# Kernel optimization log

Measured on AMD Instinct MI355X. Metric: run time of the kernel, lower is better.

Reference implementation:

```python
import jax, jax.numpy as jnp
import numpy as np

N_KERNELS = 11
B, Q, D, E, C = 128, 32, 512, 300, 128

def _kernel_mus(n):
    mus = [1.0]
    bs = 2.0 / (n - 1)
    mus.append(1 - bs / 2)
    for i in range(1, n - 1):
        mus.append(mus[i] - bs)
    return np.array(mus, dtype=np.float32)

def _kernel_sigmas(n):
    bs = 2.0 / (n - 1)
    return np.array([0.001] + [0.5 * bs] * (n - 1), dtype=np.float32)

def setup_inputs():
    key = jax.random.key(0)
    ks = jax.random.split(key, 10)
    return {
        "query_embeddings": jax.random.normal(ks[0], (B, Q, E), jnp.float32),
        "document_embeddings": jax.random.normal(ks[1], (B, D, E), jnp.float32),
        "query_pad_oov_mask": jnp.ones((B, Q), jnp.float32),
        "document_pad_oov_mask": jnp.ones((B, D), jnp.float32),
        "conv1_w": jax.random.normal(ks[2], (C, E, 1), jnp.float32) * 0.05,
        "conv1_b": jnp.zeros((C,), jnp.float32),
        "conv2_w": jax.random.normal(ks[3], (C, E, 2), jnp.float32) * 0.05,
        "conv2_b": jnp.zeros((C,), jnp.float32),
        "conv3_w": jax.random.normal(ks[4], (C, E, 3), jnp.float32) * 0.05,
        "conv3_b": jnp.zeros((C,), jnp.float32),
        "nn_scaler": jnp.full((1,), 0.01, jnp.float32),
        "dense_w": jax.random.uniform(ks[5], (1, N_KERNELS * 9), jnp.float32, -0.014, 0.014),
        "dense_b": jnp.zeros((1,), jnp.float32),
        "dense_mean_w": jax.random.normal(ks[6], (1, N_KERNELS * 9), jnp.float32) * 0.05,
        "dense_mean_b": jnp.zeros((1,), jnp.float32),
        "dense_comb_w": jax.random.normal(ks[7], (1, 2), jnp.float32) * 0.5,
    }

def _conv_relu(x, w, b):
    # x: [B, L, E] -> [B, L, C]; right-pad by k-1 (ConstantPad1d((0, k-1))) so out len == L
    k = w.shape[-1]
    y = jax.lax.conv_general_dilated(x.transpose(0, 2, 1), w, (1,), [(0, k - 1)],
                                     dimension_numbers=("NCH", "OIH", "NCH"))
    return jax.nn.relu(y + b[None, :, None]).transpose(0, 2, 1)

def _kernel_pool(q, d, qd_mask, q_mask, doc_len, mu, sigma, scaler):
    # cosine matrix (AllenNLP CosineMatrixAttention: L2-normalize with 1e-13 tie-break)
    qn = q / (jnp.linalg.norm(q, axis=-1, keepdims=True) + 1e-13)
    dn = d / (jnp.linalg.norm(d, axis=-1, keepdims=True) + 1e-13)
    cos = jnp.einsum("bqc,bdc->bqd", qn, dn) * qd_mask
    # RBF soft-histogram kernels over the similarity matrix: [B,q,d,K]
    kr = jnp.exp(-(cos[..., None] - mu) ** 2 / (2.0 * sigma ** 2)) * qd_mask[..., None]
    pkq = kr.sum(axis=2)  # [B, Q, K]
    std = (jnp.log(jnp.clip(pkq, 1e-10)) * scaler * q_mask[..., None]).sum(axis=1)
    pkq_mean = pkq / doc_len[:, None, None]
    mean = (jnp.log(jnp.clip(pkq_mean, 1e-10)) * scaler * q_mask[..., None]).sum(axis=1)
    return std, mean

def _forward(qe, de, qm, dm, c1w, c1b, c2w, c2b, c3w, c3b, ns, dw, db, dmw, dmb, dcw):
    mu = jnp.asarray(_kernel_mus(N_KERNELS))
    sigma = jnp.asarray(_kernel_sigmas(N_KERNELS))
    qd_mask = qm[:, :, None] * dm[:, None, :]
    doc_len = dm.sum(axis=1)
    convs = [(c1w, c1b), (c2w, c2b), (c3w, c3b)]
    q_res = [_conv_relu(qe, w, b) for w, b in convs]
    d_res = [_conv_relu(de, w, b) for w, b in convs]
    std_list, mean_list = [], []
    for qr in q_res:
        for dr in d_res:
            s, m = _kernel_pool(qr, dr, qd_mask, qm, doc_len, mu, sigma, ns)
            std_list.append(s)
            mean_list.append(m)
    all_grams = jnp.concatenate(std_list, axis=1)       # [B, 9*K]
    all_grams_mean = jnp.concatenate(mean_list, axis=1)
    dense_out = all_grams @ dw.T + db
    dense_mean_out = all_grams_mean @ dmw.T + dmb
    comb = jnp.concatenate([dense_out, dense_mean_out], axis=1) @ dcw.T
    return comb[:, 0]

def reference(query_embeddings, document_embeddings, query_pad_oov_mask, document_pad_oov_mask,
              conv1_w, conv1_b, conv2_w, conv2_b, conv3_w, conv3_b,
              nn_scaler, dense_w, dense_b, dense_mean_w, dense_mean_b, dense_comb_w):
    return _forward(query_embeddings, document_embeddings, query_pad_oov_mask, document_pad_oov_mask,
                    conv1_w, conv1_b, conv2_w, conv2_b, conv3_w, conv3_b,
                    nn_scaler, dense_w, dense_b, dense_mean_w, dense_mean_b, dense_comb_w)
```

## Files before the change

kernel.cpp:

```cpp
#include <hip/hip_runtime.h>
#include <hip/hip_bf16.h>
#include <cstdint>

namespace {

typedef __bf16 bf8v __attribute__((ext_vector_type(8)));
typedef __bf16 bf4v __attribute__((ext_vector_type(4)));
typedef float  f4v  __attribute__((ext_vector_type(4)));

constexpr int kB = 128;
constexpr int kQ = 32;
constexpr int kD = 512;
constexpr int kE = 300;
constexpr int kC = 128;
constexpr int kK = 11;

constexpr size_t QNB_B = 491520;
constexpr size_t DNB_B = 3637248;
constexpr size_t PKQ_B = 53968896;

constexpr float LOG2E = 1.4426950408889634f;

constexpr int XS_STRIDE = 344;

__global__ __launch_bounds__(256) void prep_kernel(
    const float* __restrict__ w1, const float* __restrict__ w2, const float* __restrict__ w3,
    __bf16* __restrict__ wb)
{
  int i = blockIdx.x * 256 + threadIdx.x;
  if (i >= 245760) return;
  int el = i & 31;
  int sc = i >> 5;
  int c  = sc & 127;
  int sk = sc >> 7;
  int slab = sk / 10;
  int ks = sk - slab * 10;
  int e = ks * 32 + el;
  float v = 0.f;
  if (e < kE) {
    if (slab == 0)      v = w1[c * kE + e];
    else if (slab <= 2) v = w2[(c * kE + e) * 2 + (slab - 1)];
    else                v = w3[(c * kE + e) * 3 + (slab - 3)];
  }
  wb[i] = (__bf16)v;
}

template<int NJ, int SLAB0>
__device__ __forceinline__ void conv_grp(
    const __bf16* __restrict__ wb, const __bf16* __restrict__ Xs,
    int lr, int g, int wm, int wn, f4v (&acc)[2][4])
{
  constexpr int N = NJ * 10;
  const __bf16* wl = wb + (size_t)SLAB0 * 10 * 4096 + (size_t)(wn * 64 + lr) * 32 + g * 8;
  const int arow = wm * 32 + lr;
  const int ae   = g * 8;

  bf8v W[3][4];
  bf8v A[2][2];
  #pragma unroll
  for (int nf = 0; nf < 4; ++nf) W[0][nf] = *(const bf8v*)(wl + nf * 512);
  #pragma unroll
  for (int nf = 0; nf < 4; ++nf) W[1][nf] = *(const bf8v*)(wl + 4096 + nf * 512);
  #pragma unroll
  for (int mf = 0; mf < 2; ++mf)
    A[0][mf] = *(const bf8v*)&Xs[(arow + mf * 16) * XS_STRIDE + ae];

  #pragma unroll
  for (int sg = 0; sg < N; ++sg) {
    const int cur = sg % 3, nxt = (sg + 2) % 3, ca = sg & 1;
    if (sg + 2 < N) {
      #pragma unroll
      for (int nf = 0; nf < 4; ++nf)
        W[nxt][nf] = *(const bf8v*)(wl + (size_t)(sg + 2) * 4096 + nf * 512);
    }
    if (sg + 1 < N) {
      const int j1 = (sg + 1) / 10, ks1 = (sg + 1) % 10;
      #pragma unroll
      for (int mf = 0; mf < 2; ++mf)
        A[ca ^ 1][mf] = *(const bf8v*)&Xs[(arow + j1 + mf * 16) * XS_STRIDE + ks1 * 32 + ae];
    }
    #pragma unroll
    for (int nf = 0; nf < 4; ++nf) {
      acc[0][nf] = __builtin_amdgcn_mfma_f32_16x16x32_bf16(A[ca][0], W[cur][nf], acc[0][nf], 0, 0, 0);
      acc[1][nf] = __builtin_amdgcn_mfma_f32_16x16x32_bf16(A[ca][1], W[cur][nf], acc[1][nf], 0, 0, 0);
    }
  }
}

__global__ __launch_bounds__(256, 3) void conv_fused(
    const float* __restrict__ qe, const float* __restrict__ de,
    const __bf16* __restrict__ wb,
    const float* __restrict__ b1, const float* __restrict__ b2, const float* __restrict__ b3,
    __bf16* __restrict__ qnb, __bf16* __restrict__ dnb)
{
  const int bx = blockIdx.x;
  const int b  = blockIdx.y;
  const bool isq = (bx == 0);
  const int L  = isq ? kQ : kD;
  const int p0 = isq ? 0 : (bx - 1) * 64;
  const float* xsrc = (isq ? qe : de) + (size_t)b * L * kE;

  const int t = threadIdx.x;
  const int w = t >> 6, l = t & 63;
  const int wm = w & 1, wn = w >> 1;
  const int lr = l & 15, g = l >> 4;

  __shared__ __align__(16) __bf16 Xs[66 * XS_STRIDE];
  __shared__ float sqs[2][64];

  for (int idx = t; idx < 66 * 82; idx += 256) {
    int row = idx / 82, c4 = idx - row * 82;
    int gp = p0 + row;
    float4 v = make_float4(0.f, 0.f, 0.f, 0.f);
    if (gp < L && c4 < 75) v = *(const float4*)(xsrc + (size_t)gp * kE + c4 * 4);
    bf4v hv = { (__bf16)v.x, (__bf16)v.y, (__bf16)v.z, (__bf16)v.w };
    *(bf4v*)&Xs[row * XS_STRIDE + c4 * 4] = hv;
  }
  __syncthreads();

  #pragma unroll
  for (int grp = 0; grp < 3; ++grp) {
    f4v acc[2][4];
    #pragma unroll
    for (int mf = 0; mf < 2; ++mf)
      #pragma unroll
      for (int nf = 0; nf < 4; ++nf)
        acc[mf][nf] = (f4v)0.f;

    if (grp == 0)      conv_grp<1, 0>(wb, Xs, lr, g, wm, wn, acc);
    else if (grp == 1) conv_grp<2, 1>(wb, Xs, lr, g, wm, wn, acc);
    else               conv_grp<3, 3>(wb, Xs, lr, g, wm, wn, acc);

    const float* bias = (grp == 0) ? b1 : ((grp == 1) ? b2 : b3);
    float bvs[4];
    #pragma unroll
    for (int nf = 0; nf < 4; ++nf) bvs[nf] = bias[wn * 64 + nf * 16 + lr];

    f4v ssum[2];
    #pragma unroll
    for (int mf = 0; mf < 2; ++mf) {
      ssum[mf] = (f4v)0.f;
      #pragma unroll
      for (int nf = 0; nf < 4; ++nf)
        #pragma unroll
        for (int r = 0; r < 4; ++r) {
          float y = fmaxf(acc[mf][nf][r] + bvs[nf], 0.f);
          acc[mf][nf][r] = y;
          ssum[mf][r] += y * y;
        }
    }
    #pragma unroll
    for (int off = 1; off < 16; off <<= 1)
      #pragma unroll
      for (int mf = 0; mf < 2; ++mf)
        #pragma unroll
        for (int r = 0; r < 4; ++r)
          ssum[mf][r] += __shfl_xor(ssum[mf][r], off);

    __syncthreads();
    if (lr == 0) {
      #pragma unroll
      for (int mf = 0; mf < 2; ++mf)
        *(float4*)&sqs[wn][wm * 32 + mf * 16 + g * 4] = *(float4*)&ssum[mf];
    }
    __syncthreads();
    f4v inv[2];
    #pragma unroll
    for (int mf = 0; mf < 2; ++mf) {
      float4 o = *(const float4*)&sqs[1 - wn][wm * 32 + mf * 16 + g * 4];
      inv[mf][0] = 1.f / (sqrtf(ssum[mf][0] + o.x) + 1e-13f);
      inv[mf][1] = 1.f / (sqrtf(ssum[mf][1] + o.y) + 1e-13f);
      inv[mf][2] = 1.f / (sqrtf(ssum[mf][2] + o.z) + 1e-13f);
      inv[mf][3] = 1.f / (sqrtf(ssum[mf][3] + o.w) + 1e-13f);
    }
    __bf16* outp = (isq ? qnb : dnb) + ((size_t)(grp * kB + b)) * L * kC;
    #pragma unroll
    for (int mf = 0; mf < 2; ++mf) {
      #pragma unroll
      for (int r = 0; r < 4; ++r) {
        int gp = p0 + wm * 32 + mf * 16 + g * 4 + r;
        if (gp < L) {
          #pragma unroll
          for (int nf = 0; nf < 4; ++nf) {
            int c = wn * 64 + nf * 16 + lr;
            outp[(size_t)gp * kC + c] = (__bf16)(acc[mf][nf][r] * inv[mf][r]);
          }
        }
      }
    }
  }
}

__global__ __launch_bounds__(256) void pool_mfma(
    const __bf16* __restrict__ qnb,
    const __bf16* __restrict__ dnb,
    const float* __restrict__ qmask,
    const float* __restrict__ dmask,
    float* __restrict__ pkq)
{
  const int pair = blockIdx.x;
  const int b = blockIdx.y;
  const int qi = pair / 3, dj = pair - qi * 3;
  const __bf16* qb = qnb + ((size_t)qi * kB + b) * kQ * kC;
  const __bf16* db = dnb + ((size_t)dj * kB + b) * kD * kC;

  const int t = threadIdx.x;
  const int w = t >> 6, l = t & 63;
  const int lr = l & 15, g = l >> 4;

  __shared__ float red[4][2][16][kK];

  bf8v Bq[2][4];
  #pragma unroll
  for (int qt = 0; qt < 2; ++qt)
    #pragma unroll
    for (int kc = 0; kc < 4; ++kc)
      Bq[qt][kc] = *(const bf8v*)&qb[(size_t)(qt * 16 + lr) * kC + kc * 32 + g * 8];

  float qmv[2];
  #pragma unroll
  for (int qt = 0; qt < 2; ++qt) qmv[qt] = qmask[b * kQ + qt * 16 + lr];

  const float c1[10] = { 129.84255368f, 100.98865286f,  72.13475204f,  43.28085123f,  14.42695041f,
                         -14.42695041f, -43.28085123f, -72.13475204f, -100.98865286f, -129.84255368f };
  const float c2[10] = { -58.42914915f, -35.34602850f, -18.03368801f, -6.49212768f, -0.72134752f,
                          -0.72134752f,  -6.49212768f, -18.03368801f, -35.34602850f, -58.42914915f };
  const float C50 = -50.f * LOG2E;
  const float C0  = -500000.f * LOG2E;

  float pk[2][kK];
  #pragma unroll
  for (int qt = 0; qt < 2; ++qt)
    #pragma unroll
    for (int k = 0; k < kK; ++k) pk[qt][k] = 0.f;

  const int dt0 = w * 8;
  bf8v An[4];
  #pragma unroll
  for (int kc = 0; kc < 4; ++kc)
    An[kc] = *(const bf8v*)&db[(size_t)(dt0 * 16 + lr) * kC + kc * 32 + g * 8];

  for (int dtl = 0; dtl < 8; ++dtl) {
    const int drow0 = (dt0 + dtl) * 16;
    bf8v Ac[4];
    #pragma unroll
    for (int kc = 0; kc < 4; ++kc) Ac[kc] = An[kc];
    if (dtl < 7) {
      #pragma unroll
      for (int kc = 0; kc < 4; ++kc)
        An[kc] = *(const bf8v*)&db[(size_t)(drow0 + 16 + lr) * kC + kc * 32 + g * 8];
    }
    f4v acc0 = (f4v)0.f, acc1 = (f4v)0.f;
    #pragma unroll
    for (int kc = 0; kc < 4; ++kc) {
      acc0 = __builtin_amdgcn_mfma_f32_16x16x32_bf16(Ac[kc], Bq[0][kc], acc0, 0, 0, 0);
      acc1 = __builtin_amdgcn_mfma_f32_16x16x32_bf16(Ac[kc], Bq[1][kc], acc1, 0, 0, 0);
    }
    float4 dmv = *(const float4*)&dmask[b * kD + drow0 + g * 4];
    #pragma unroll
    for (int qt = 0; qt < 2; ++qt) {
      const f4v& a = qt ? acc1 : acc0;
      #pragma unroll
      for (int r = 0; r < 4; ++r) {
        float dm = (r == 0) ? dmv.x : (r == 1) ? dmv.y : (r == 2) ? dmv.z : dmv.w;
        float off = fmaf(dm, 1000.f, -1000.f);
        float s = a[r] * qmv[qt] * dm;
        float s2 = s * s;
        float base = fmaf(s2, C50, off);
        float dd = s - 1.f;
        pk[qt][0] += exp2f(fmaf(dd * dd, C0, off));
        #pragma unroll
        for (int k = 0; k < 10; ++k)
          pk[qt][k + 1] += exp2f(fmaf(c1[k], s, base) + c2[k]);
      }
    }
  }

  #pragma unroll
  for (int off = 16; off < 64; off <<= 1)
    #pragma unroll
    for (int qt = 0; qt < 2; ++qt)
      #pragma unroll
      for (int k = 0; k < kK; ++k)
        pk[qt][k] += __shfl_xor(pk[qt][k], off);

  if (l < 16) {
    #pragma unroll
    for (int qt = 0; qt < 2; ++qt)
      #pragma unroll
      for (int k = 0; k < kK; ++k)
        red[w][qt][lr][k] = pk[qt][k];
  }
  __syncthreads();
  for (int i = t; i < 2 * 16 * kK; i += 256) {
    int qt = i / (16 * kK);
    int rem = i - qt * 16 * kK;
    int lq = rem / kK, k = rem - lq * kK;
    float v = red[0][qt][lq][k] + red[1][qt][lq][k] + red[2][qt][lq][k] + red[3][qt][lq][k];
    int q = qt * 16 + lq;
    pkq[(((size_t)pair * kB + b) * kQ + q) * kK + k] = v * qmask[b * kQ + q];
  }
}

__global__ __launch_bounds__(128) void finalize_kernel(
    const float* __restrict__ pkq, const float* __restrict__ qmask,
    const float* __restrict__ dmask, const float* __restrict__ nsp,
    const float* __restrict__ dw, const float* __restrict__ dbp,
    const float* __restrict__ dmw, const float* __restrict__ dmbp,
    const float* __restrict__ dcw, float* __restrict__ out)
{
  const int b = blockIdx.x;
  const int t = threadIdx.x;
  __shared__ float sh[4];
  float dl = 0.f;
  for (int d = t; d < kD; d += 128) dl += dmask[b * kD + d];
  #pragma unroll
  for (int off = 1; off < 64; off <<= 1) dl += __shfl_xor(dl, off);
  if ((t & 63) == 0) sh[t >> 6] = dl;
  __syncthreads();
  const float idl = 1.f / (sh[0] + sh[1]);
  const float sc = nsp[0];
  float ps = 0.f, pm = 0.f;
  for (int i = t; i < 99; i += 128) {
    int pr = i / kK, kk = i - pr * kK;
    const float* base = pkq + ((size_t)pr * kB + b) * kQ * kK + kk;
    float ss = 0.f, sm = 0.f;
    for (int q = 0; q < kQ; ++q) {
      float v = base[q * kK];
      float qq = qmask[b * kQ + q];
      ss += __logf(fmaxf(v, 1e-10f)) * qq;
      sm += __logf(fmaxf(v * idl, 1e-10f)) * qq;
    }
    ps += dw[i] * ss;
    pm += dmw[i] * sm;
  }
  ps *= sc; pm *= sc;
  #pragma unroll
  for (int off = 1; off < 64; off <<= 1) { ps += __shfl_xor(ps, off); pm += __shfl_xor(pm, off); }
  __syncthreads();
  if ((t & 63) == 0) { sh[t >> 6] = ps; sh[2 + (t >> 6)] = pm; }
  __syncthreads();
  if (t == 0) {
    float PS = sh[0] + sh[1] + dbp[0];
    float PM = sh[2] + sh[3] + dmbp[0];
    out[b] = dcw[0] * PS + dcw[1] * PM;
  }
}

}

extern "C" void kernel_launch(void* const* d_in, const int* in_sizes, int n_in,
                              void* d_out, int out_size, void* d_ws, size_t ws_size,
                              hipStream_t stream) {
  const float* qe  = (const float*)d_in[0];
  const float* de  = (const float*)d_in[1];
  const float* qm  = (const float*)d_in[2];
  const float* dm  = (const float*)d_in[3];
  const float* w1  = (const float*)d_in[4];
  const float* b1  = (const float*)d_in[5];
  const float* w2  = (const float*)d_in[6];
  const float* b2  = (const float*)d_in[7];
  const float* w3  = (const float*)d_in[8];
  const float* b3  = (const float*)d_in[9];
  const float* ns  = (const float*)d_in[10];
  const float* dw  = (const float*)d_in[11];
  const float* db  = (const float*)d_in[12];
  const float* dmw = (const float*)d_in[13];
  const float* dmb = (const float*)d_in[14];
  const float* dcw = (const float*)d_in[15];
  float* out = (float*)d_out;

  char* wsb = (char*)d_ws;
  __bf16* wb  = (__bf16*)wsb;
  __bf16* qnb = (__bf16*)(wsb + QNB_B);
  __bf16* dnb = (__bf16*)(wsb + DNB_B);
  float*  pkq = (float*)(wsb + PKQ_B);

  prep_kernel<<<960, 256, 0, stream>>>(w1, w2, w3, wb);
  conv_fused<<<dim3(9, kB), 256, 0, stream>>>(qe, de, wb, b1, b2, b3, qnb, dnb);
  pool_mfma<<<dim3(9, kB), 256, 0, stream>>>(qnb, dnb, qm, dm, pkq);
  finalize_kernel<<<kB, 128, 0, stream>>>(pkq, qm, dm, ns, dw, db, dmw, dmb, dcw, out);
}
```

Measured before the change: 183.0 us.

## Stage conv weights into LDS via async global_load_lds with swizzled layout

Conv weight chunks are now double-buffered into shared memory with direct global-to-LDS loads instead of each wave loading them into registers from global memory. The weight prep kernel applies an XOR swizzle so the LDS reads avoid bank conflicts, and the Xs row stride is reduced. This cuts the redundant global weight traffic per block and the register pressure, but adds a __syncthreads per K-step and more LDS use, and occupancy is lowered from 3 to 2 blocks per CU.

```diff
diff --git a/kernel.cpp b/kernel.cpp
--- a/kernel.cpp
+++ b/kernel.cpp
@@ -21,7 +21,7 @@
 
 constexpr float LOG2E = 1.4426950408889634f;
 
-constexpr int XS_STRIDE = 344;
+constexpr int XS_STRIDE = 336;
 
 __global__ __launch_bounds__(256) void prep_kernel(
     const float* __restrict__ w1, const float* __restrict__ w2, const float* __restrict__ w3,
@@ -29,13 +29,15 @@
 {
   int i = blockIdx.x * 256 + threadIdx.x;
   if (i >= 245760) return;
-  int el = i & 31;
-  int sc = i >> 5;
-  int c  = sc & 127;
-  int sk = sc >> 7;
-  int slab = sk / 10;
-  int ks = sk - slab * 10;
-  int e = ks * 32 + el;
+  int e8   = i & 7;
+  int sg   = i >> 3;
+  int slot = sg & 511;
+  int chunk = sg >> 9;
+  int c  = slot >> 2;
+  int gq = (slot & 3) ^ ((slot >> 3) & 3);
+  int slab = chunk / 10;
+  int ks = chunk - slab * 10;
+  int e = ks * 32 + gq * 8 + e8;
   float v = 0.f;
   if (e < kE) {
     if (slab == 0)      v = w1[c * kE + e];
@@ -45,49 +47,58 @@
   wb[i] = (__bf16)v;
 }
 
-template<int NJ, int SLAB0>
+__device__ __forceinline__ void stage_chunk(const __bf16* __restrict__ gchunk,
+                                            __bf16* __restrict__ ldst, int w, int l) {
+  const __bf16* g0 = gchunk + (size_t)(w * 128 + l) * 8;
+  const __bf16* g1 = gchunk + (size_t)(w * 128 + 64 + l) * 8;
+  __bf16* l0 = ldst + w * 1024;
+  __bf16* l1 = ldst + w * 1024 + 512;
+  __builtin_amdgcn_global_load_lds(
+      (const __attribute__((address_space(1))) uint32_t*)g0,
+      (__attribute__((address_space(3))) uint32_t*)l0, 16, 0, 0);
+  __builtin_amdgcn_global_load_lds(
+      (const __attribute__((address_space(1))) uint32_t*)g1,
+      (__attribute__((address_space(3))) uint32_t*)l1, 16, 0, 0);
+}
+
+template<int NJ, int CH0>
 __device__ __forceinline__ void conv_grp(
     const __bf16* __restrict__ wb, const __bf16* __restrict__ Xs,
-    int lr, int g, int wm, int wn, f4v (&acc)[2][4])
+    __bf16* __restrict__ Wb0, __bf16* __restrict__ Wb1,
+    int w, int l, int lr, int g, int wm, int wn, f4v (&acc)[2][4])
 {
   constexpr int N = NJ * 10;
-  const __bf16* wl = wb + (size_t)SLAB0 * 10 * 4096 + (size_t)(wn * 64 + lr) * 32 + g * 8;
+  const int wboff = (wn * 64 + lr) * 32 + (g ^ ((lr >> 1) & 3)) * 8;
   const int arow = wm * 32 + lr;
-  const int ae   = g * 8;
-
-  bf8v W[3][4];
-  bf8v A[2][2];
-  #pragma unroll
-  for (int nf = 0; nf < 4; ++nf) W[0][nf] = *(const bf8v*)(wl + nf * 512);
-  #pragma unroll
-  for (int nf = 0; nf < 4; ++nf) W[1][nf] = *(const bf8v*)(wl + 4096 + nf * 512);
-  #pragma unroll
-  for (int mf = 0; mf < 2; ++mf)
-    A[0][mf] = *(const bf8v*)&Xs[(arow + mf * 16) * XS_STRIDE + ae];
-
-  #pragma unroll
-  for (int sg = 0; sg < N; ++sg) {
-    const int cur = sg % 3, nxt = (sg + 2) % 3, ca = sg & 1;
-    if (sg + 2 < N) {
-      #pragma unroll
-      for (int nf = 0; nf < 4; ++nf)
-        W[nxt][nf] = *(const bf8v*)(wl + (size_t)(sg + 2) * 4096 + nf * 512);
-    }
-    if (sg + 1 < N) {
-      const int j1 = (sg + 1) / 10, ks1 = (sg + 1) % 10;
-      #pragma unroll
-      for (int mf = 0; mf < 2; ++mf)
-        A[ca ^ 1][mf] = *(const bf8v*)&Xs[(arow + j1 + mf * 16) * XS_STRIDE + ks1 * 32 + ae];
-    }
-    #pragma unroll
-    for (int nf = 0; nf < 4; ++nf) {
-      acc[0][nf] = __builtin_amdgcn_mfma_f32_16x16x32_bf16(A[ca][0], W[cur][nf], acc[0][nf], 0, 0, 0);
-      acc[1][nf] = __builtin_amdgcn_mfma_f32_16x16x32_bf16(A[ca][1], W[cur][nf], acc[1][nf], 0, 0, 0);
-    }
-  }
-}
-
-__global__ __launch_bounds__(256, 3) void conv_fused(
+  const int ae = g * 8;
+
+  #pragma unroll
+  for (int sgi = 0; sgi < N; ++sgi) {
+    const int chunk = CH0 + sgi;
+    __bf16* cur = (chunk & 1) ? Wb1 : Wb0;
+    __bf16* nxt = (chunk & 1) ? Wb0 : Wb1;
+    if (chunk + 1 < 60)
+      stage_chunk(wb + (size_t)(chunk + 1) * 4096, nxt, w, l);
+    const int j = sgi / 10, ks = sgi - (sgi / 10) * 10;
+    bf8v A0 = *(const bf8v*)&Xs[(arow + j) * XS_STRIDE + ks * 32 + ae];
+    bf8v A1 = *(const bf8v*)&Xs[(arow + j + 16) * XS_STRIDE + ks * 32 + ae];
+    bf8v W0 = *(const bf8v*)(cur + wboff);
+    bf8v W1 = *(const bf8v*)(cur + wboff + 512);
+    bf8v W2 = *(const bf8v*)(cur + wboff + 1024);
+    bf8v W3 = *(const bf8v*)(cur + wboff + 1536);
+    acc[0][0] = __builtin_amdgcn_mfma_f32_16x16x32_bf16(A0, W0, acc[0][0], 0, 0, 0);
+    acc[1][0] = __builtin_amdgcn_mfma_f32_16x16x32_bf16(A1, W0, acc[1][0], 0, 0, 0);
+    acc[0][1] = __builtin_amdgcn_mfma_f32_16x16x32_bf16(A0, W1, acc[0][1], 0, 0, 0);
+    acc[1][1] = __builtin_amdgcn_mfma_f32_16x16x32_bf16(A1, W1, acc[1][1], 0, 0, 0);
+    acc[0][2] = __builtin_amdgcn_mfma_f32_16x16x32_bf16(A0, W2, acc[0][2], 0, 0, 0);
+    acc[1][2] = __builtin_amdgcn_mfma_f32_16x16x32_bf16(A1, W2, acc[1][2], 0, 0, 0);
+    acc[0][3] = __builtin_amdgcn_mfma_f32_16x16x32_bf16(A0, W3, acc[0][3], 0, 0, 0);
+    acc[1][3] = __builtin_amdgcn_mfma_f32_16x16x32_bf16(A1, W3, acc[1][3], 0, 0, 0);
+    __syncthreads();
+  }
+}
+
+__global__ __launch_bounds__(256, 2) void conv_fused(
     const float* __restrict__ qe, const float* __restrict__ de,
     const __bf16* __restrict__ wb,
     const float* __restrict__ b1, const float* __restrict__ b2, const float* __restrict__ b3,
@@ -106,8 +117,10 @@
   const int lr = l & 15, g = l >> 4;
 
   __shared__ __align__(16) __bf16 Xs[66 * XS_STRIDE];
+  __shared__ __align__(16) __bf16 Wbuf[2][4096];
   __shared__ float sqs[2][64];
 
+  stage_chunk(wb, &Wbuf[0][0], w, l);
   for (int idx = t; idx < 66 * 82; idx += 256) {
     int row = idx / 82, c4 = idx - row * 82;
     int gp = p0 + row;
@@ -127,9 +140,9 @@
       for (int nf = 0; nf < 4; ++nf)
         acc[mf][nf] = (f4v)0.f;
 
-    if (grp == 0)      conv_grp<1, 0>(wb, Xs, lr, g, wm, wn, acc);
-    else if (grp == 1) conv_grp<2, 1>(wb, Xs, lr, g, wm, wn, acc);
-    else               conv_grp<3, 3>(wb, Xs, lr, g, wm, wn, acc);
+    if (grp == 0)      conv_grp<1, 0>(wb, Xs, &Wbuf[0][0], &Wbuf[1][0], w, l, lr, g, wm, wn, acc);
+    else if (grp == 1) conv_grp<2, 10>(wb, Xs, &Wbuf[0][0], &Wbuf[1][0], w, l, lr, g, wm, wn, acc);
+    else               conv_grp<3, 30>(wb, Xs, &Wbuf[0][0], &Wbuf[1][0], w, l, lr, g, wm, wn, acc);
 
     const float* bias = (grp == 0) ? b1 : ((grp == 1) ? b2 : b3);
     float bvs[4];
@@ -173,6 +186,7 @@
       inv[mf][2] = 1.f / (sqrtf(ssum[mf][2] + o.z) + 1e-13f);
       inv[mf][3] = 1.f / (sqrtf(ssum[mf][3] + o.w) + 1e-13f);
     }
+    __syncthreads();
     __bf16* outp = (isq ? qnb : dnb) + ((size_t)(grp * kB + b)) * L * kC;
     #pragma unroll
     for (int mf = 0; mf < 2; ++mf) {
```

Measured after the change: 176.4 us. 3.6% less time.
